# Optimization experiments

Hardware: AMD Instinct MI355X
Metric: run time of the kernel (lower is better)

Reference implementation:

```python
import jax, jax.numpy as jnp
import numpy as np
from jax import lax


def _conv3x3(x, w, b):
    # x: [B,C,H,W], w: [O,I,3,3] -> SAME padding, stride 1 (matches nn.Conv2d(.,.,3,1,1))
    y = lax.conv_general_dilated(x, w, window_strides=(1, 1), padding='SAME',
                                 dimension_numbers=('NCHW', 'OIHW', 'NCHW'))
    return y + b[None, :, None, None]


def _smooth_mask(h, w, dtype=jnp.float32):
    # Mirrors create_smooth_mask: torch.meshgrid(x, y, indexing='xy') -> shape (h, w),
    # xx varies along width, yy along height.
    yv = jnp.linspace(0.0, 1.0, h, dtype=dtype)   # height coords
    xv = jnp.linspace(0.0, 1.0, w, dtype=dtype)   # width coords
    xx = jnp.broadcast_to(xv[None, :], (h, w))
    yy = jnp.broadcast_to(yv[:, None], (h, w))
    edge_falloff = 0.1
    def edge(t):
        return jnp.minimum(jax.nn.sigmoid((t - edge_falloff) / 0.1),
                           jax.nn.sigmoid((1.0 - t - edge_falloff) / 0.1))
    return edge(xx) * edge(yy)  # (h, w); channel repeat handled by broadcasting


def _kaiming(key, shape):
    # kaiming_normal_(mode='fan_out', nonlinearity='relu'): std = sqrt(2 / fan_out)
    fan_out = shape[0] * shape[2] * shape[3]
    return jax.random.normal(key, shape, dtype=jnp.float32) * np.sqrt(2.0 / fan_out).astype(np.float32)


def setup_inputs() -> dict:
    key = jax.random.key(0)
    ks = jax.random.split(key, 6)
    B, H, W = 4, 720, 1280
    return {
        'frame1': jax.random.normal(ks[0], (B, 3, H, W), dtype=jnp.float32),
        'frame3': jax.random.normal(ks[1], (B, 3, H, W), dtype=jnp.float32),
        'w1': _kaiming(ks[2], (32, 6, 3, 3)),  'b1': jnp.zeros((32,), jnp.float32),
        'w2': _kaiming(ks[3], (48, 32, 3, 3)), 'b2': jnp.zeros((48,), jnp.float32),
        'w3': _kaiming(ks[4], (32, 48, 3, 3)), 'b3': jnp.zeros((32,), jnp.float32),
        'w4': _kaiming(ks[5], (3, 32, 3, 3)),  'b4': jnp.zeros((3,), jnp.float32),
    }


def reference(frame1, frame3, w1, b1, w2, b2, w3, b3, w4, b4):
    # For these inputs the detected motion region is the full frame for every
    # batch element (see notes), so the per-region loop batches into one pass.
    B, C, H, W = frame1.shape
    avg = (frame1 + frame3) * 0.5
    x = jnp.concatenate([frame1, frame3], axis=1)          # [B,6,H,W]
    h = jax.nn.relu(_conv3x3(x, w1, b1))                   # [B,32,H,W]
    h = jax.nn.relu(_conv3x3(h, w2, b2))                   # [B,48,H,W]
    h = jax.nn.relu(_conv3x3(h, w3, b3))                   # [B,32,H,W]
    region_out = _conv3x3(h, w4, b4)                       # [B,3,H,W]
    mask = _smooth_mask(H, W, frame1.dtype)[None, None]    # [1,1,H,W]
    out = avg * (1.0 - mask) + region_out * mask
    return jnp.clip(out, -1.0, 1.0)
```

## Files before the change

kernel.cpp:

```cpp
#include <hip/hip_runtime.h>

#define BATCH 4
#define H 720
#define W 1280
#define HW (H*W)

typedef _Float16 f16x8 __attribute__((ext_vector_type(8)));
typedef __attribute__((ext_vector_type(4))) float f32x4;

#define WP1_B 0
#define WP2_B 8192
#define WP3A_B 40960
#define WP3B_B 61440
#define WP4_B 81920
#define WP_BYTES 98304

__device__ __forceinline__ ushort f2h(float x) {
    union { _Float16 h; ushort u; } c; c.h = (_Float16)x; return c.u;
}

__global__ void pack_x_kernel(const float* __restrict__ f1, const float* __restrict__ f3,
                              ushort* __restrict__ X,
                              int xr0, int rows_x, int xbase, int RBX) {
    int p = blockIdx.x * 256 + threadIdx.x;
    int npix = BATCH * rows_x * W;
    if (p >= npix) return;
    int b = p / (rows_x * W);
    int rem = p - b * (rows_x * W);
    int ri = rem / W;
    int col = rem - ri * W;
    int img_row = xr0 + ri;
    int buf_row = img_row - xbase;
    const float* p1 = f1 + (size_t)b * 3 * HW + (size_t)img_row * W + col;
    const float* p3 = f3 + (size_t)b * 3 * HW + (size_t)img_row * W + col;
    union { ushort u[8]; uint4 v; } r;
    r.u[0] = f2h(p1[0]);  r.u[1] = f2h(p1[HW]);  r.u[2] = f2h(p1[2*HW]);
    r.u[3] = f2h(p3[0]);  r.u[4] = f2h(p3[HW]);  r.u[5] = f2h(p3[2*HW]);
    r.u[6] = 0; r.u[7] = 0;
    *reinterpret_cast<uint4*>(X + (((size_t)b * RBX + buf_row) * W + col) * 8) = r.v;
}

__global__ void pack_w_kernel(const float* __restrict__ w1, const float* __restrict__ w2,
                              const float* __restrict__ w3, const float* __restrict__ w4,
                              ushort* __restrict__ wp1, ushort* __restrict__ wp2,
                              ushort* __restrict__ wp3a, ushort* __restrict__ wp3b,
                              ushort* __restrict__ wp4) {
    int i = blockIdx.x * 256 + threadIdx.x;
    if (i < 3072) {
        int j = i & 7, l = (i >> 3) & 63, f = i >> 9;
        int dy = f >> 1, mt = f & 1;
        int dx = l >> 4, ci = j, och = mt * 16 + (l & 15);
        float v = 0.f;
        if (dx < 3 && ci < 6) v = w1[((och * 6 + ci) * 3 + dy) * 3 + dx];
        wp1[i] = f2h(v);
        return;
    }
    i -= 3072;
    if (i < 13824) {
        int j = i & 7, l = (i >> 3) & 63, f = i >> 9;
        int tap = f / 3, mt = f - tap * 3;
        int dy = tap / 3, dx = tap - dy * 3;
        int och = mt * 16 + (l & 15), ci = (l >> 4) * 8 + j;
        wp2[i] = f2h(w2[((och * 32 + ci) * 3 + dy) * 3 + dx]);
        return;
    }
    i -= 13824;
    if (i < 9216) {
        int j = i & 7, l = (i >> 3) & 63, f = i >> 9;
        int tap = f >> 1, mt = f & 1;
        int dy = tap / 3, dx = tap - dy * 3;
        int och = mt * 16 + (l & 15), ci = (l >> 4) * 8 + j;
        wp3a[i] = f2h(w3[((och * 48 + ci) * 3 + dy) * 3 + dx]);
        return;
    }
    i -= 9216;
    if (i < 9216) {
        int j = i & 7, l = (i >> 3) & 63, f = i >> 9;
        int tap = f >> 1, mt = f & 1;
        int dy = tap / 3, dx = tap - dy * 3;
        int och = mt * 16 + (l & 15), ci = 32 + (l >> 4) * 8 + j;
        float v = 0.f;
        if (ci < 48) v = w3[((och * 48 + ci) * 3 + dy) * 3 + dx];
        wp3b[i] = f2h(v);
        return;
    }
    i -= 9216;
    if (i < 4608) {
        int j = i & 7, l = (i >> 3) & 63, tap = i >> 9;
        int dy = tap / 3, dx = tap - dy * 3;
        int och = l & 15, ci = (l >> 4) * 8 + j;
        float v = 0.f;
        if (och < 3) v = w4[((och * 32 + ci) * 3 + dy) * 3 + dx];
        wp4[i] = f2h(v);
    }
}

__device__ __forceinline__ void lds_copy(const unsigned char* __restrict__ g, char* s, int bytes) {
    const uint4* gs = reinterpret_cast<const uint4*>(g);
    uint4* ss = reinterpret_cast<uint4*>(s);
    for (int i = threadIdx.x; i < bytes / 16; i += 256) ss[i] = gs[i];
    __syncthreads();
}

__global__ __launch_bounds__(256) void conv1_kernel(const ushort* __restrict__ Xg,
                                                    const float* __restrict__ bias,
                                                    ushort* __restrict__ Y,
                                                    const unsigned char* __restrict__ wp,
                                                    int y0, int xbase, int RBX, int y1base, int RBY1) {
    __shared__ char lds[6144];
    lds_copy(wp, lds, 6144);
    int wave = threadIdx.x >> 6, lane = threadIdx.x & 63;
    int l15 = lane & 15, lhi = lane >> 4;
    int y = y0 + blockIdx.y, b = blockIdx.z;
    int x0 = blockIdx.x * 256 + wave * 64;

    f32x4 acc[2][4] = {};
    #pragma unroll
    for (int dy = 0; dy < 3; ++dy) {
        int yy = y + dy - 1;
        bool rv = (yy >= 0 && yy < H);
        size_t srow = ((size_t)b * RBX + (yy - xbase)) * W;
        f16x8 bfrag[4];
        #pragma unroll
        for (int nt = 0; nt < 4; ++nt) {
            int xc = x0 + nt * 16 + l15 + lhi - 1;
            uint4 v = make_uint4(0, 0, 0, 0);
            if (rv && lhi < 3 && xc >= 0 && xc < W)
                v = *reinterpret_cast<const uint4*>(Xg + (srow + xc) * 8);
            bfrag[nt] = *reinterpret_cast<f16x8*>(&v);
        }
        #pragma unroll
        for (int mt = 0; mt < 2; ++mt) {
            f16x8 a = *reinterpret_cast<f16x8*>(lds + ((dy * 2 + mt) * 64 + lane) * 16);
            #pragma unroll
            for (int nt = 0; nt < 4; ++nt)
                acc[mt][nt] = __builtin_amdgcn_mfma_f32_16x16x32_f16(a, bfrag[nt], acc[mt][nt], 0, 0, 0);
        }
    }
    size_t drow = ((size_t)b * RBY1 + (y - y1base)) * W;
    #pragma unroll
    for (int mt = 0; mt < 2; ++mt) {
        float4 bs = *reinterpret_cast<const float4*>(bias + mt * 16 + lhi * 4);
        const float* bsp = reinterpret_cast<const float*>(&bs);
        #pragma unroll
        for (int nt = 0; nt < 4; ++nt) {
            size_t pix = drow + x0 + nt * 16 + l15;
            ushort o[4];
            #pragma unroll
            for (int r = 0; r < 4; ++r) o[r] = f2h(fmaxf(acc[mt][nt][r] + bsp[r], 0.f));
            *reinterpret_cast<uint2*>(Y + pix * 32 + mt * 16 + lhi * 4) = *reinterpret_cast<uint2*>(o);
        }
    }
}

__global__ __launch_bounds__(256) void conv2_kernel(const ushort* __restrict__ Y1,
                                                    const float* __restrict__ bias,
                                                    ushort* __restrict__ Y2,
                                                    const unsigned char* __restrict__ wp,
                                                    int y0, int y1base, int RBY1, int y2base, int RBY2) {
    __shared__ char lds[27648];
    lds_copy(wp, lds, 27648);
    int wave = threadIdx.x >> 6, lane = threadIdx.x & 63;
    int l15 = lane & 15, lhi = lane >> 4;
    int y = y0 + blockIdx.y, b = blockIdx.z;
    int x0 = blockIdx.x * 256 + wave * 64;

    f32x4 acc[3][4] = {};
    #pragma unroll
    for (int dy = 0; dy < 3; ++dy) {
        int yy = y + dy - 1;
        bool rv = (yy >= 0 && yy < H);
        size_t srow = ((size_t)b * RBY1 + (yy - y1base)) * W;
        #pragma unroll
        for (int dx = 0; dx < 3; ++dx) {
            int tap = dy * 3 + dx;
            f16x8 bfrag[4];
            #pragma unroll
            for (int nt = 0; nt < 4; ++nt) {
                int xc = x0 + nt * 16 + l15 + dx - 1;
                uint4 v = make_uint4(0, 0, 0, 0);
                if (rv && xc >= 0 && xc < W)
                    v = *reinterpret_cast<const uint4*>(Y1 + (srow + xc) * 32 + lhi * 8);
                bfrag[nt] = *reinterpret_cast<f16x8*>(&v);
            }
            #pragma unroll
            for (int mt = 0; mt < 3; ++mt) {
                f16x8 a = *reinterpret_cast<f16x8*>(lds + ((tap * 3 + mt) * 64 + lane) * 16);
                #pragma unroll
                for (int nt = 0; nt < 4; ++nt)
                    acc[mt][nt] = __builtin_amdgcn_mfma_f32_16x16x32_f16(a, bfrag[nt], acc[mt][nt], 0, 0, 0);
            }
        }
    }
    size_t drow = ((size_t)b * RBY2 + (y - y2base)) * W;
    #pragma unroll
    for (int mt = 0; mt < 3; ++mt) {
        float4 bs = *reinterpret_cast<const float4*>(bias + mt * 16 + lhi * 4);
        const float* bsp = reinterpret_cast<const float*>(&bs);
        #pragma unroll
        for (int nt = 0; nt < 4; ++nt) {
            size_t pix = drow + x0 + nt * 16 + l15;
            ushort o[4];
            #pragma unroll
            for (int r = 0; r < 4; ++r) o[r] = f2h(fmaxf(acc[mt][nt][r] + bsp[r], 0.f));
            *reinterpret_cast<uint2*>(Y2 + pix * 48 + mt * 16 + lhi * 4) = *reinterpret_cast<uint2*>(o);
        }
    }
}

__global__ __launch_bounds__(256) void conv3_kernel(const ushort* __restrict__ Y2,
                                                    const float* __restrict__ bias,
                                                    ushort* __restrict__ Y3,
                                                    const unsigned char* __restrict__ wpa,
                                                    const unsigned char* __restrict__ wpb,
                                                    int y0, int y2base, int RBY2, int y3base, int RBY3) {
    __shared__ char lds[36864];
    {
        const uint4* ga = reinterpret_cast<const uint4*>(wpa);
        const uint4* gb = reinterpret_cast<const uint4*>(wpb);
        uint4* ss = reinterpret_cast<uint4*>(lds);
        for (int i = threadIdx.x; i < 18432 / 16; i += 256) { ss[i] = ga[i]; ss[i + 1152] = gb[i]; }
        __syncthreads();
    }
    int wave = threadIdx.x >> 6, lane = threadIdx.x & 63;
    int l15 = lane & 15, lhi = lane >> 4;
    int y = y0 + blockIdx.y, b = blockIdx.z;
    int x0 = blockIdx.x * 256 + wave * 64;

    f32x4 acc[2][4] = {};
    #pragma unroll
    for (int dy = 0; dy < 3; ++dy) {
        int yy = y + dy - 1;
        bool rv = (yy >= 0 && yy < H);
        size_t srow = ((size_t)b * RBY2 + (yy - y2base)) * W;
        #pragma unroll
        for (int dx = 0; dx < 3; ++dx) {
            int tap = dy * 3 + dx;
            f16x8 b0[4], b1[4];
            #pragma unroll
            for (int nt = 0; nt < 4; ++nt) {
                int xc = x0 + nt * 16 + l15 + dx - 1;
                bool valid = rv && xc >= 0 && xc < W;
                uint4 v0 = make_uint4(0, 0, 0, 0), v1 = make_uint4(0, 0, 0, 0);
                if (valid)
                    v0 = *reinterpret_cast<const uint4*>(Y2 + (srow + xc) * 48 + lhi * 8);
                if (valid && lhi < 2)
                    v1 = *reinterpret_cast<const uint4*>(Y2 + (srow + xc) * 48 + 32 + lhi * 8);
                b0[nt] = *reinterpret_cast<f16x8*>(&v0);
                b1[nt] = *reinterpret_cast<f16x8*>(&v1);
            }
            #pragma unroll
            for (int mt = 0; mt < 2; ++mt) {
                f16x8 a0 = *reinterpret_cast<f16x8*>(lds + ((tap * 2 + mt) * 64 + lane) * 16);
                f16x8 a1 = *reinterpret_cast<f16x8*>(lds + 18432 + ((tap * 2 + mt) * 64 + lane) * 16);
                #pragma unroll
                for (int nt = 0; nt < 4; ++nt) {
                    acc[mt][nt] = __builtin_amdgcn_mfma_f32_16x16x32_f16(a0, b0[nt], acc[mt][nt], 0, 0, 0);
                    acc[mt][nt] = __builtin_amdgcn_mfma_f32_16x16x32_f16(a1, b1[nt], acc[mt][nt], 0, 0, 0);
                }
            }
        }
    }
    size_t drow = ((size_t)b * RBY3 + (y - y3base)) * W;
    #pragma unroll
    for (int mt = 0; mt < 2; ++mt) {
        float4 bs = *reinterpret_cast<const float4*>(bias + mt * 16 + lhi * 4);
        const float* bsp = reinterpret_cast<const float*>(&bs);
        #pragma unroll
        for (int nt = 0; nt < 4; ++nt) {
            size_t pix = drow + x0 + nt * 16 + l15;
            ushort o[4];
            #pragma unroll
            for (int r = 0; r < 4; ++r) o[r] = f2h(fmaxf(acc[mt][nt][r] + bsp[r], 0.f));
            *reinterpret_cast<uint2*>(Y3 + pix * 32 + mt * 16 + lhi * 4) = *reinterpret_cast<uint2*>(o);
        }
    }
}

__device__ __forceinline__ float edgef(float t) {
    float a = 1.f / (1.f + expf(-(t - 0.1f) * 10.f));
    float c = 1.f / (1.f + expf(-(0.9f - t) * 10.f));
    return fminf(a, c);
}

__global__ __launch_bounds__(256) void conv4_kernel(const ushort* __restrict__ Y3,
                                                    const float* __restrict__ b4,
                                                    const float* __restrict__ f1,
                                                    const float* __restrict__ f3,
                                                    float* __restrict__ out,
                                                    const unsigned char* __restrict__ wp,
                                                    int y0, int y3base, int RBY3) {
    __shared__ char lds[9216];
    lds_copy(wp, lds, 9216);
    int wave = threadIdx.x >> 6, lane = threadIdx.x & 63;
    int l15 = lane & 15, lhi = lane >> 4;
    int y = y0 + blockIdx.y, b = blockIdx.z;
    int x0 = blockIdx.x * 256 + wave * 64;

    f32x4 acc[4] = {};
    #pragma unroll
    for (int dy = 0; dy < 3; ++dy) {
        int yy = y + dy - 1;
        bool rv = (yy >= 0 && yy < H);
        size_t srow = ((size_t)b * RBY3 + (yy - y3base)) * W;
        #pragma unroll
        for (int dx = 0; dx < 3; ++dx) {
            int tap = dy * 3 + dx;
            f16x8 bfrag[4];
            #pragma unroll
            for (int nt = 0; nt < 4; ++nt) {
                int xc = x0 + nt * 16 + l15 + dx - 1;
                uint4 v = make_uint4(0, 0, 0, 0);
                if (rv && xc >= 0 && xc < W)
                    v = *reinterpret_cast<const uint4*>(Y3 + (srow + xc) * 32 + lhi * 8);
                bfrag[nt] = *reinterpret_cast<f16x8*>(&v);
            }
            f16x8 a = *reinterpret_cast<f16x8*>(lds + (tap * 64 + lane) * 16);
            #pragma unroll
            for (int nt = 0; nt < 4; ++nt)
                acc[nt] = __builtin_amdgcn_mfma_f32_16x16x32_f16(a, bfrag[nt], acc[nt], 0, 0, 0);
        }
    }
    if (lhi == 0) {
        float bv0 = b4[0], bv1 = b4[1], bv2 = b4[2];
        float ty = (float)y * (1.f / (H - 1));
        float ey = edgef(ty);
        #pragma unroll
        for (int nt = 0; nt < 4; ++nt) {
            int x = x0 + nt * 16 + l15;
            float tx = (float)x * (1.f / (W - 1));
            float m = edgef(tx) * ey;
            float om = 1.f - m;
            #pragma unroll
            for (int r = 0; r < 3; ++r) {
                float bv = (r == 0) ? bv0 : (r == 1 ? bv1 : bv2);
                size_t idx = ((size_t)(b * 3 + r) * H + y) * W + x;
                float avg = 0.5f * (f1[idx] + f3[idx]);
                float v = avg * om + (acc[nt][r] + bv) * m;
                out[idx] = fminf(fmaxf(v, -1.f), 1.f);
            }
        }
    }
}

extern "C" void kernel_launch(void* const* d_in, const int* in_sizes, int n_in,
                              void* d_out, int out_size, void* d_ws, size_t ws_size,
                              hipStream_t stream) {
    const float* f1 = (const float*)d_in[0];
    const float* f3 = (const float*)d_in[1];
    const float* w1 = (const float*)d_in[2];
    const float* b1 = (const float*)d_in[3];
    const float* w2 = (const float*)d_in[4];
    const float* b2 = (const float*)d_in[5];
    const float* w3 = (const float*)d_in[6];
    const float* b3 = (const float*)d_in[7];
    const float* w4 = (const float*)d_in[8];
    const float* b4 = (const float*)d_in[9];
    float* out = (float*)d_out;

    long avail = (long)ws_size - 131072;
    int RB = -1;
    for (int nb = 1; nb <= 180; ++nb) {
        int rb = (H + nb - 1) / nb;
        long need = 10240L * (120L * rb + 512);
        if (need <= avail) { RB = rb; break; }
    }
    if (RB < 0) return;

    int RBX = RB + 8, RBY1 = RB + 6, RBY2 = RB + 4, RBY3 = RB + 2;
    char* ws = (char*)d_ws;
    size_t offX  = 0;
    size_t offY1 = offX  + (size_t)BATCH * RBX  * W * 8  * 2;
    size_t offY2 = offY1 + (size_t)BATCH * RBY1 * W * 32 * 2;
    size_t offY3 = offY2 + (size_t)BATCH * RBY2 * W * 48 * 2;
    size_t offWP = offY3 + (size_t)BATCH * RBY3 * W * 32 * 2;
    ushort* X  = (ushort*)(ws + offX);
    ushort* Y1 = (ushort*)(ws + offY1);
    ushort* Y2 = (ushort*)(ws + offY2);
    ushort* Y3 = (ushort*)(ws + offY3);
    ushort* wp1  = (ushort*)(ws + offWP + WP1_B);
    ushort* wp2  = (ushort*)(ws + offWP + WP2_B);
    ushort* wp3a = (ushort*)(ws + offWP + WP3A_B);
    ushort* wp3b = (ushort*)(ws + offWP + WP3B_B);
    ushort* wp4  = (ushort*)(ws + offWP + WP4_B);

    pack_w_kernel<<<156, 256, 0, stream>>>(w1, w2, w3, w4, wp1, wp2, wp3a, wp3b, wp4);

    for (int r0 = 0; r0 < H; r0 += RB) {
        int r1 = r0 + RB; if (r1 > H) r1 = H;
        int xbase = r0 - 4, y1base = r0 - 3, y2base = r0 - 2, y3base = r0 - 1;

        int xr0 = r0 - 4 < 0 ? 0 : r0 - 4;
        int xr1 = r1 + 4 > H ? H : r1 + 4;
        int rows_x = xr1 - xr0;
        int npix = BATCH * rows_x * W;
        pack_x_kernel<<<(npix + 255) / 256, 256, 0, stream>>>(f1, f3, X, xr0, rows_x, xbase, RBX);

        int y10 = r0 - 3 < 0 ? 0 : r0 - 3;
        int y11 = r1 + 3 > H ? H : r1 + 3;
        conv1_kernel<<<dim3(W / 256, y11 - y10, BATCH), 256, 0, stream>>>(
            X, b1, Y1, (const unsigned char*)wp1, y10, xbase, RBX, y1base, RBY1);

        int y20 = r0 - 2 < 0 ? 0 : r0 - 2;
        int y21 = r1 + 2 > H ? H : r1 + 2;
        conv2_kernel<<<dim3(W / 256, y21 - y20, BATCH), 256, 0, stream>>>(
            Y1, b2, Y2, (const unsigned char*)wp2, y20, y1base, RBY1, y2base, RBY2);

        int y30 = r0 - 1 < 0 ? 0 : r0 - 1;
        int y31 = r1 + 1 > H ? H : r1 + 1;
        conv3_kernel<<<dim3(W / 256, y31 - y30, BATCH), 256, 0, stream>>>(
            Y2, b3, Y3, (const unsigned char*)wp3a, (const unsigned char*)wp3b,
            y30, y2base, RBY2, y3base, RBY3);

        conv4_kernel<<<dim3(W / 256, r1 - r0, BATCH), 256, 0, stream>>>(
            Y3, b4, f1, f3, out, (const unsigned char*)wp4, r0, y3base, RBY3);
    }
}
```

Measured before the change: 938.8 us.

## Pad activation buffers with zero borders, remap workgroups per XCD, hoist tap loads

Activation buffers get explicit zero-padded columns, and out-of-image rows are written as zeros. The conv kernels can then drop per-tap bounds checks and branchy loads and use plain vector loads from a single base pointer. Workgroups are flattened into a 1D grid and remapped so that contiguous work lands on the same XCD, which should improve L2 locality. Loads for all three dx taps are hoisted per dy row. The change adds a pad-zeroing kernel, extra rows of compute at the image edges, and higher register pressure from the hoisted fragments.

```diff
diff --git a/kernel.cpp b/kernel.cpp
--- a/kernel.cpp
+++ b/kernel.cpp
@@ -4,14 +4,15 @@
 #define H 720
 #define W 1280
 #define HW (H*W)
+#define WX (W+4)
+#define WP (W+2)
 
 typedef _Float16 f16x8 __attribute__((ext_vector_type(8)));
 typedef __attribute__((ext_vector_type(4))) float f32x4;
 
 #define WP1_B 0
 #define WP2_B 8192
-#define WP3A_B 40960
-#define WP3B_B 61440
+#define WP3_B 40960
 #define WP4_B 81920
 #define WP_BYTES 98304
 
@@ -19,32 +20,80 @@
     union { _Float16 h; ushort u; } c; c.h = (_Float16)x; return c.u;
 }
 
+__device__ __forceinline__ int xcd_work(int id, int nwg) {
+    int q = nwg >> 3, r = nwg & 7;
+    int k = id & 7, i = id >> 3;
+    int extra = k < r ? k : r;
+    return k * q + extra + i;
+}
+
+__global__ void zero_pads_kernel(ushort* __restrict__ X, ushort* __restrict__ Y1,
+                                 ushort* __restrict__ Y2, ushort* __restrict__ Y3,
+                                 int RBX, int RBY1, int RBY2, int RBY3) {
+    int i = blockIdx.x * 256 + threadIdx.x;
+    uint4 z = make_uint4(0, 0, 0, 0);
+    int nX = BATCH * RBX * 4;
+    if (i < nX) {
+        int c4 = i & 3, row = i >> 2;
+        int col = (c4 == 0) ? 0 : (W + c4);
+        *reinterpret_cast<uint4*>(X + ((size_t)row * WX + col) * 8) = z;
+        return;
+    }
+    i -= nX;
+    int n1 = BATCH * RBY1 * 2;
+    if (i < n1) {
+        int c = i & 1, row = i >> 1;
+        int col = c ? (W + 1) : 0;
+        uint4* p = reinterpret_cast<uint4*>(Y1 + ((size_t)row * WP + col) * 32);
+        p[0] = z; p[1] = z; p[2] = z; p[3] = z;
+        return;
+    }
+    i -= n1;
+    int n2 = BATCH * RBY2 * 2;
+    if (i < n2) {
+        int c = i & 1, row = i >> 1;
+        int col = c ? (W + 1) : 0;
+        uint4* p = reinterpret_cast<uint4*>(Y2 + ((size_t)row * WP + col) * 48);
+        p[0] = z; p[1] = z; p[2] = z; p[3] = z; p[4] = z; p[5] = z;
+        return;
+    }
+    i -= n2;
+    int n3 = BATCH * RBY3 * 2;
+    if (i < n3) {
+        int c = i & 1, row = i >> 1;
+        int col = c ? (W + 1) : 0;
+        uint4* p = reinterpret_cast<uint4*>(Y3 + ((size_t)row * WP + col) * 32);
+        p[0] = z; p[1] = z; p[2] = z; p[3] = z;
+    }
+}
+
 __global__ void pack_x_kernel(const float* __restrict__ f1, const float* __restrict__ f3,
-                              ushort* __restrict__ X,
-                              int xr0, int rows_x, int xbase, int RBX) {
+                              ushort* __restrict__ X, int xbase, int RBX) {
     int p = blockIdx.x * 256 + threadIdx.x;
-    int npix = BATCH * rows_x * W;
+    int npix = BATCH * RBX * W;
     if (p >= npix) return;
-    int b = p / (rows_x * W);
-    int rem = p - b * (rows_x * W);
+    int b = p / (RBX * W);
+    int rem = p - b * (RBX * W);
     int ri = rem / W;
     int col = rem - ri * W;
-    int img_row = xr0 + ri;
-    int buf_row = img_row - xbase;
-    const float* p1 = f1 + (size_t)b * 3 * HW + (size_t)img_row * W + col;
-    const float* p3 = f3 + (size_t)b * 3 * HW + (size_t)img_row * W + col;
+    int img_row = xbase + ri;
     union { ushort u[8]; uint4 v; } r;
-    r.u[0] = f2h(p1[0]);  r.u[1] = f2h(p1[HW]);  r.u[2] = f2h(p1[2*HW]);
-    r.u[3] = f2h(p3[0]);  r.u[4] = f2h(p3[HW]);  r.u[5] = f2h(p3[2*HW]);
-    r.u[6] = 0; r.u[7] = 0;
-    *reinterpret_cast<uint4*>(X + (((size_t)b * RBX + buf_row) * W + col) * 8) = r.v;
+    if (img_row >= 0 && img_row < H) {
+        const float* p1 = f1 + (size_t)b * 3 * HW + (size_t)img_row * W + col;
+        const float* p3 = f3 + (size_t)b * 3 * HW + (size_t)img_row * W + col;
+        r.u[0] = f2h(p1[0]);  r.u[1] = f2h(p1[HW]);  r.u[2] = f2h(p1[2*HW]);
+        r.u[3] = f2h(p3[0]);  r.u[4] = f2h(p3[HW]);  r.u[5] = f2h(p3[2*HW]);
+        r.u[6] = 0; r.u[7] = 0;
+    } else {
+        r.v = make_uint4(0, 0, 0, 0);
+    }
+    *reinterpret_cast<uint4*>(X + (((size_t)b * RBX + ri) * WX + col + 1) * 8) = r.v;
 }
 
 __global__ void pack_w_kernel(const float* __restrict__ w1, const float* __restrict__ w2,
                               const float* __restrict__ w3, const float* __restrict__ w4,
                               ushort* __restrict__ wp1, ushort* __restrict__ wp2,
-                              ushort* __restrict__ wp3a, ushort* __restrict__ wp3b,
-                              ushort* __restrict__ wp4) {
+                              ushort* __restrict__ wp3, ushort* __restrict__ wp4) {
     int i = blockIdx.x * 256 + threadIdx.x;
     if (i < 3072) {
         int j = i & 7, l = (i >> 3) & 63, f = i >> 9;
@@ -70,7 +119,7 @@
         int tap = f >> 1, mt = f & 1;
         int dy = tap / 3, dx = tap - dy * 3;
         int och = mt * 16 + (l & 15), ci = (l >> 4) * 8 + j;
-        wp3a[i] = f2h(w3[((och * 48 + ci) * 3 + dy) * 3 + dx]);
+        wp3[i] = f2h(w3[((och * 48 + ci) * 3 + dy) * 3 + dx]);
         return;
     }
     i -= 9216;
@@ -81,7 +130,7 @@
         int och = mt * 16 + (l & 15), ci = 32 + (l >> 4) * 8 + j;
         float v = 0.f;
         if (ci < 48) v = w3[((och * 48 + ci) * 3 + dy) * 3 + dx];
-        wp3b[i] = f2h(v);
+        wp3[9216 + i] = f2h(v);
         return;
     }
     i -= 9216;
@@ -106,29 +155,26 @@
                                                     const float* __restrict__ bias,
                                                     ushort* __restrict__ Y,
                                                     const unsigned char* __restrict__ wp,
-                                                    int y0, int xbase, int RBX, int y1base, int RBY1) {
+                                                    int y0, int ny, int xbase, int RBX,
+                                                    int y1base, int RBY1) {
     __shared__ char lds[6144];
     lds_copy(wp, lds, 6144);
     int wave = threadIdx.x >> 6, lane = threadIdx.x & 63;
     int l15 = lane & 15, lhi = lane >> 4;
-    int y = y0 + blockIdx.y, b = blockIdx.z;
-    int x0 = blockIdx.x * 256 + wave * 64;
+    int work = xcd_work(blockIdx.x, gridDim.x);
+    int bx = work % 5, t = work / 5, by = t % ny, b = t / ny;
+    int y = y0 + by;
+    int x0 = bx * 256 + wave * 64;
+    bool zrow = (y < 0) | (y >= H);
 
     f32x4 acc[2][4] = {};
     #pragma unroll
     for (int dy = 0; dy < 3; ++dy) {
-        int yy = y + dy - 1;
-        bool rv = (yy >= 0 && yy < H);
-        size_t srow = ((size_t)b * RBX + (yy - xbase)) * W;
+        const ushort* rp = Xg + (((size_t)b * RBX + (y + dy - 1 - xbase)) * WX + x0 + l15 + lhi) * 8;
         f16x8 bfrag[4];
         #pragma unroll
-        for (int nt = 0; nt < 4; ++nt) {
-            int xc = x0 + nt * 16 + l15 + lhi - 1;
-            uint4 v = make_uint4(0, 0, 0, 0);
-            if (rv && lhi < 3 && xc >= 0 && xc < W)
-                v = *reinterpret_cast<const uint4*>(Xg + (srow + xc) * 8);
-            bfrag[nt] = *reinterpret_cast<f16x8*>(&v);
-        }
+        for (int nt = 0; nt < 4; ++nt)
+            bfrag[nt] = *reinterpret_cast<const f16x8*>(rp + nt * 128);
         #pragma unroll
         for (int mt = 0; mt < 2; ++mt) {
             f16x8 a = *reinterpret_cast<f16x8*>(lds + ((dy * 2 + mt) * 64 + lane) * 16);
@@ -137,18 +183,18 @@
                 acc[mt][nt] = __builtin_amdgcn_mfma_f32_16x16x32_f16(a, bfrag[nt], acc[mt][nt], 0, 0, 0);
         }
     }
-    size_t drow = ((size_t)b * RBY1 + (y - y1base)) * W;
+    ushort* wpx = Y + (((size_t)b * RBY1 + (y - y1base)) * WP + x0 + l15 + 1) * 32 + lhi * 4;
     #pragma unroll
     for (int mt = 0; mt < 2; ++mt) {
         float4 bs = *reinterpret_cast<const float4*>(bias + mt * 16 + lhi * 4);
         const float* bsp = reinterpret_cast<const float*>(&bs);
         #pragma unroll
         for (int nt = 0; nt < 4; ++nt) {
-            size_t pix = drow + x0 + nt * 16 + l15;
             ushort o[4];
             #pragma unroll
-            for (int r = 0; r < 4; ++r) o[r] = f2h(fmaxf(acc[mt][nt][r] + bsp[r], 0.f));
-            *reinterpret_cast<uint2*>(Y + pix * 32 + mt * 16 + lhi * 4) = *reinterpret_cast<uint2*>(o);
+            for (int r = 0; r < 4; ++r)
+                o[r] = zrow ? (ushort)0 : f2h(fmaxf(acc[mt][nt][r] + bsp[r], 0.f));
+            *reinterpret_cast<uint2*>(wpx + nt * 512 + mt * 16) = *reinterpret_cast<uint2*>(o);
         }
     }
 }
@@ -157,53 +203,51 @@
                                                     const float* __restrict__ bias,
                                                     ushort* __restrict__ Y2,
                                                     const unsigned char* __restrict__ wp,
-                                                    int y0, int y1base, int RBY1, int y2base, int RBY2) {
+                                                    int y0, int ny, int y1base, int RBY1,
+                                                    int y2base, int RBY2) {
     __shared__ char lds[27648];
     lds_copy(wp, lds, 27648);
     int wave = threadIdx.x >> 6, lane = threadIdx.x & 63;
     int l15 = lane & 15, lhi = lane >> 4;
-    int y = y0 + blockIdx.y, b = blockIdx.z;
-    int x0 = blockIdx.x * 256 + wave * 64;
+    int work = xcd_work(blockIdx.x, gridDim.x);
+    int bx = work % 5, t = work / 5, by = t % ny, b = t / ny;
+    int y = y0 + by;
+    int x0 = bx * 256 + wave * 64;
+    bool zrow = (y < 0) | (y >= H);
+    int c0 = x0 + l15;
 
     f32x4 acc[3][4] = {};
     #pragma unroll
     for (int dy = 0; dy < 3; ++dy) {
-        int yy = y + dy - 1;
-        bool rv = (yy >= 0 && yy < H);
-        size_t srow = ((size_t)b * RBY1 + (yy - y1base)) * W;
-        #pragma unroll
-        for (int dx = 0; dx < 3; ++dx) {
-            int tap = dy * 3 + dx;
-            f16x8 bfrag[4];
-            #pragma unroll
-            for (int nt = 0; nt < 4; ++nt) {
-                int xc = x0 + nt * 16 + l15 + dx - 1;
-                uint4 v = make_uint4(0, 0, 0, 0);
-                if (rv && xc >= 0 && xc < W)
-                    v = *reinterpret_cast<const uint4*>(Y1 + (srow + xc) * 32 + lhi * 8);
-                bfrag[nt] = *reinterpret_cast<f16x8*>(&v);
-            }
+        const ushort* rp = Y1 + (((size_t)b * RBY1 + (y + dy - 1 - y1base)) * WP + c0) * 32 + lhi * 8;
+        f16x8 bf[3][4];
+        #pragma unroll
+        for (int nt = 0; nt < 4; ++nt)
+            #pragma unroll
+            for (int dx = 0; dx < 3; ++dx)
+                bf[dx][nt] = *reinterpret_cast<const f16x8*>(rp + nt * 512 + dx * 32);
+        #pragma unroll
+        for (int dx = 0; dx < 3; ++dx)
             #pragma unroll
             for (int mt = 0; mt < 3; ++mt) {
-                f16x8 a = *reinterpret_cast<f16x8*>(lds + ((tap * 3 + mt) * 64 + lane) * 16);
+                f16x8 a = *reinterpret_cast<f16x8*>(lds + (((dy * 3 + dx) * 3 + mt) * 64 + lane) * 16);
                 #pragma unroll
                 for (int nt = 0; nt < 4; ++nt)
-                    acc[mt][nt] = __builtin_amdgcn_mfma_f32_16x16x32_f16(a, bfrag[nt], acc[mt][nt], 0, 0, 0);
-            }
-        }
-    }
-    size_t drow = ((size_t)b * RBY2 + (y - y2base)) * W;
+                    acc[mt][nt] = __builtin_amdgcn_mfma_f32_16x16x32_f16(a, bf[dx][nt], acc[mt][nt], 0, 0, 0);
+            }
+    }
+    ushort* wpx = Y2 + (((size_t)b * RBY2 + (y - y2base)) * WP + x0 + l15 + 1) * 48 + lhi * 4;
     #pragma unroll
     for (int mt = 0; mt < 3; ++mt) {
         float4 bs = *reinterpret_cast<const float4*>(bias + mt * 16 + lhi * 4);
         const float* bsp = reinterpret_cast<const float*>(&bs);
         #pragma unroll
         for (int nt = 0; nt < 4; ++nt) {
-            size_t pix = drow + x0 + nt * 16 + l15;
             ushort o[4];
             #pragma unroll
-            for (int r = 0; r < 4; ++r) o[r] = f2h(fmaxf(acc[mt][nt][r] + bsp[r], 0.f));
-            *reinterpret_cast<uint2*>(Y2 + pix * 48 + mt * 16 + lhi * 4) = *reinterpret_cast<uint2*>(o);
+            for (int r = 0; r < 4; ++r)
+                o[r] = zrow ? (ushort)0 : f2h(fmaxf(acc[mt][nt][r] + bsp[r], 0.f));
+            *reinterpret_cast<uint2*>(wpx + nt * 768 + mt * 16) = *reinterpret_cast<uint2*>(o);
         }
     }
 }
@@ -211,68 +255,71 @@
 __global__ __launch_bounds__(256) void conv3_kernel(const ushort* __restrict__ Y2,
                                                     const float* __restrict__ bias,
                                                     ushort* __restrict__ Y3,
-                                                    const unsigned char* __restrict__ wpa,
-                                                    const unsigned char* __restrict__ wpb,
-                                                    int y0, int y2base, int RBY2, int y3base, int RBY3) {
+                                                    const unsigned char* __restrict__ wp,
+                                                    int y0, int ny, int y2base, int RBY2,
+                                                    int y3base, int RBY3) {
     __shared__ char lds[36864];
-    {
-        const uint4* ga = reinterpret_cast<const uint4*>(wpa);
-        const uint4* gb = reinterpret_cast<const uint4*>(wpb);
-        uint4* ss = reinterpret_cast<uint4*>(lds);
-        for (int i = threadIdx.x; i < 18432 / 16; i += 256) { ss[i] = ga[i]; ss[i + 1152] = gb[i]; }
-        __syncthreads();
-    }
+    lds_copy(wp, lds, 36864);
     int wave = threadIdx.x >> 6, lane = threadIdx.x & 63;
     int l15 = lane & 15, lhi = lane >> 4;
-    int y = y0 + blockIdx.y, b = blockIdx.z;
-    int x0 = blockIdx.x * 256 + wave * 64;
+    int work = xcd_work(blockIdx.x, gridDim.x);
+    int bx = work % 5, t = work / 5, by = t % ny, b = t / ny;
+    int y = y0 + by;
+    int x0 = bx * 256 + wave * 64;
+    bool zrow = (y < 0) | (y >= H);
+    int c0 = x0 + l15;
 
     f32x4 acc[2][4] = {};
     #pragma unroll
     for (int dy = 0; dy < 3; ++dy) {
-        int yy = y + dy - 1;
-        bool rv = (yy >= 0 && yy < H);
-        size_t srow = ((size_t)b * RBY2 + (yy - y2base)) * W;
-        #pragma unroll
-        for (int dx = 0; dx < 3; ++dx) {
-            int tap = dy * 3 + dx;
-            f16x8 b0[4], b1[4];
-            #pragma unroll
-            for (int nt = 0; nt < 4; ++nt) {
-                int xc = x0 + nt * 16 + l15 + dx - 1;
-                bool valid = rv && xc >= 0 && xc < W;
-                uint4 v0 = make_uint4(0, 0, 0, 0), v1 = make_uint4(0, 0, 0, 0);
-                if (valid)
-                    v0 = *reinterpret_cast<const uint4*>(Y2 + (srow + xc) * 48 + lhi * 8);
-                if (valid && lhi < 2)
-                    v1 = *reinterpret_cast<const uint4*>(Y2 + (srow + xc) * 48 + 32 + lhi * 8);
-                b0[nt] = *reinterpret_cast<f16x8*>(&v0);
-                b1[nt] = *reinterpret_cast<f16x8*>(&v1);
-            }
+        const ushort* rp = Y2 + (((size_t)b * RBY2 + (y + dy - 1 - y2base)) * WP + c0) * 48 + lhi * 8;
+        const ushort* rp2 = rp + 1536;
+        f16x8 bf[3][4];
+        #pragma unroll
+        for (int nt = 0; nt < 2; ++nt)
+            #pragma unroll
+            for (int dx = 0; dx < 3; ++dx) {
+                bf[dx][nt]     = *reinterpret_cast<const f16x8*>(rp  + nt * 768 + dx * 48);
+                bf[dx][nt + 2] = *reinterpret_cast<const f16x8*>(rp2 + nt * 768 + dx * 48);
+            }
+        #pragma unroll
+        for (int dx = 0; dx < 3; ++dx)
             #pragma unroll
             for (int mt = 0; mt < 2; ++mt) {
-                f16x8 a0 = *reinterpret_cast<f16x8*>(lds + ((tap * 2 + mt) * 64 + lane) * 16);
-                f16x8 a1 = *reinterpret_cast<f16x8*>(lds + 18432 + ((tap * 2 + mt) * 64 + lane) * 16);
+                f16x8 a = *reinterpret_cast<f16x8*>(lds + (((dy * 3 + dx) * 2 + mt) * 64 + lane) * 16);
                 #pragma unroll
-                for (int nt = 0; nt < 4; ++nt) {
-                    acc[mt][nt] = __builtin_amdgcn_mfma_f32_16x16x32_f16(a0, b0[nt], acc[mt][nt], 0, 0, 0);
-                    acc[mt][nt] = __builtin_amdgcn_mfma_f32_16x16x32_f16(a1, b1[nt], acc[mt][nt], 0, 0, 0);
-                }
-            }
-        }
-    }
-    size_t drow = ((size_t)b * RBY3 + (y - y3base)) * W;
+                for (int nt = 0; nt < 4; ++nt)
+                    acc[mt][nt] = __builtin_amdgcn_mfma_f32_16x16x32_f16(a, bf[dx][nt], acc[mt][nt], 0, 0, 0);
+            }
+        #pragma unroll
+        for (int nt = 0; nt < 2; ++nt)
+            #pragma unroll
+            for (int dx = 0; dx < 3; ++dx) {
+                bf[dx][nt]     = *reinterpret_cast<const f16x8*>(rp  + nt * 768 + dx * 48 + 32);
+                bf[dx][nt + 2] = *reinterpret_cast<const f16x8*>(rp2 + nt * 768 + dx * 48 + 32);
+            }
+        #pragma unroll
+        for (int dx = 0; dx < 3; ++dx)
+            #pragma unroll
+            for (int mt = 0; mt < 2; ++mt) {
+                f16x8 a = *reinterpret_cast<f16x8*>(lds + 18432 + (((dy * 3 + dx) * 2 + mt) * 64 + lane) * 16);
+                #pragma unroll
+                for (int nt = 0; nt < 4; ++nt)
+                    acc[mt][nt] = __builtin_amdgcn_mfma_f32_16x16x32_f16(a, bf[dx][nt], acc[mt][nt], 0, 0, 0);
+            }
+    }
+    ushort* wpx = Y3 + (((size_t)b * RBY3 + (y - y3base)) * WP + x0 + l15 + 1) * 32 + lhi * 4;
     #pragma unroll
     for (int mt = 0; mt < 2; ++mt) {
         float4 bs = *reinterpret_cast<const float4*>(bias + mt * 16 + lhi * 4);
         const float* bsp = reinterpret_cast<const float*>(&bs);
         #pragma unroll
         for (int nt = 0; nt < 4; ++nt) {
-            size_t pix = drow + x0 + nt * 16 + l15;
             ushort o[4];
             #pragma unroll
-            for (int r = 0; r < 4; ++r) o[r] = f2h(fmaxf(acc[mt][nt][r] + bsp[r], 0.f));
-            *reinterpret_cast<uint2*>(Y3 + pix * 32 + mt * 16 + lhi * 4) = *reinterpret_cast<uint2*>(o);
+            for (int r = 0; r < 4; ++r)
+                o[r] = zrow ? (ushort)0 : f2h(fmaxf(acc[mt][nt][r] + bsp[r], 0.f));
+            *reinterpret_cast<uint2*>(wpx + nt * 512 + mt * 16) = *reinterpret_cast<uint2*>(o);
         }
     }
 }
@@ -289,36 +336,33 @@
                                                     const float* __restrict__ f3,
                                                     float* __restrict__ out,
                                                     const unsigned char* __restrict__ wp,
-                                                    int y0, int y3base, int RBY3) {
+                                                    int y0, int ny, int y3base, int RBY3) {
     __shared__ char lds[9216];
     lds_copy(wp, lds, 9216);
     int wave = threadIdx.x >> 6, lane = threadIdx.x & 63;
     int l15 = lane & 15, lhi = lane >> 4;
-    int y = y0 + blockIdx.y, b = blockIdx.z;
-    int x0 = blockIdx.x * 256 + wave * 64;
+    int work = xcd_work(blockIdx.x, gridDim.x);
+    int bx = work % 5, t = work / 5, by = t % ny, b = t / ny;
+    int y = y0 + by;
+    int x0 = bx * 256 + wave * 64;
+    int c0 = x0 + l15;
 
     f32x4 acc[4] = {};
     #pragma unroll
     for (int dy = 0; dy < 3; ++dy) {
-        int yy = y + dy - 1;
-        bool rv = (yy >= 0 && yy < H);
-        size_t srow = ((size_t)b * RBY3 + (yy - y3base)) * W;
+        const ushort* rp = Y3 + (((size_t)b * RBY3 + (y + dy - 1 - y3base)) * WP + c0) * 32 + lhi * 8;
+        f16x8 bf[3][4];
+        #pragma unroll
+        for (int nt = 0; nt < 4; ++nt)
+            #pragma unroll
+            for (int dx = 0; dx < 3; ++dx)
+                bf[dx][nt] = *reinterpret_cast<const f16x8*>(rp + nt * 512 + dx * 32);
         #pragma unroll
         for (int dx = 0; dx < 3; ++dx) {
-            int tap = dy * 3 + dx;
-            f16x8 bfrag[4];
-            #pragma unroll
-            for (int nt = 0; nt < 4; ++nt) {
-                int xc = x0 + nt * 16 + l15 + dx - 1;
-                uint4 v = make_uint4(0, 0, 0, 0);
-                if (rv && xc >= 0 && xc < W)
-                    v = *reinterpret_cast<const uint4*>(Y3 + (srow + xc) * 32 + lhi * 8);
-                bfrag[nt] = *reinterpret_cast<f16x8*>(&v);
-            }
-            f16x8 a = *reinterpret_cast<f16x8*>(lds + (tap * 64 + lane) * 16);
+            f16x8 a = *reinterpret_cast<f16x8*>(lds + ((dy * 3 + dx) * 64 + lane) * 16);
             #pragma unroll
             for (int nt = 0; nt < 4; ++nt)
-                acc[nt] = __builtin_amdgcn_mfma_f32_16x16x32_f16(a, bfrag[nt], acc[nt], 0, 0, 0);
+                acc[nt] = __builtin_amdgcn_mfma_f32_16x16x32_f16(a, bf[dx][nt], acc[nt], 0, 0, 0);
         }
     }
     if (lhi == 0) {
@@ -358,61 +402,55 @@
     const float* b4 = (const float*)d_in[9];
     float* out = (float*)d_out;
 
-    long avail = (long)ws_size - 131072;
     int RB = -1;
     for (int nb = 1; nb <= 180; ++nb) {
         int rb = (H + nb - 1) / nb;
-        long need = 10240L * (120L * rb + 512);
-        if (need <= avail) { RB = rb; break; }
+        long need = 1230848L * rb + 5252096L + 131072L;
+        if (need <= (long)ws_size) { RB = rb; break; }
     }
     if (RB < 0) return;
 
     int RBX = RB + 8, RBY1 = RB + 6, RBY2 = RB + 4, RBY3 = RB + 2;
     char* ws = (char*)d_ws;
     size_t offX  = 0;
-    size_t offY1 = offX  + (size_t)BATCH * RBX  * W * 8  * 2;
-    size_t offY2 = offY1 + (size_t)BATCH * RBY1 * W * 32 * 2;
-    size_t offY3 = offY2 + (size_t)BATCH * RBY2 * W * 48 * 2;
-    size_t offWP = offY3 + (size_t)BATCH * RBY3 * W * 32 * 2;
+    size_t offY1 = offX  + (size_t)BATCH * RBX  * WX * 8  * 2;
+    size_t offY2 = offY1 + (size_t)BATCH * RBY1 * WP * 32 * 2;
+    size_t offY3 = offY2 + (size_t)BATCH * RBY2 * WP * 48 * 2;
+    size_t offWPr = offY3 + (size_t)BATCH * RBY3 * WP * 32 * 2;
     ushort* X  = (ushort*)(ws + offX);
     ushort* Y1 = (ushort*)(ws + offY1);
     ushort* Y2 = (ushort*)(ws + offY2);
     ushort* Y3 = (ushort*)(ws + offY3);
-    ushort* wp1  = (ushort*)(ws + offWP + WP1_B);
-    ushort* wp2  = (ushort*)(ws + offWP + WP2_B);
-    ushort* wp3a = (ushort*)(ws + offWP + WP3A_B);
-    ushort* wp3b = (ushort*)(ws + offWP + WP3B_B);
-    ushort* wp4  = (ushort*)(ws + offWP + WP4_B);
-
-    pack_w_kernel<<<156, 256, 0, stream>>>(w1, w2, w3, w4, wp1, wp2, wp3a, wp3b, wp4);
+    ushort* wp1 = (ushort*)(ws + offWPr + WP1_B);
+    ushort* wp2 = (ushort*)(ws + offWPr + WP2_B);
+    ushort* wp3 = (ushort*)(ws + offWPr + WP3_B);
+    ushort* wp4 = (ushort*)(ws + offWPr + WP4_B);
+
+    pack_w_kernel<<<156, 256, 0, stream>>>(w1, w2, w3, w4, wp1, wp2, wp3, wp4);
+    int npad = BATCH * (RBX * 4 + (RBY1 + RBY2 + RBY3) * 2);
+    zero_pads_kernel<<<(npad + 255) / 256, 256, 0, stream>>>(X, Y1, Y2, Y3, RBX, RBY1, RBY2, RBY3);
 
     for (int r0 = 0; r0 < H; r0 += RB) {
         int r1 = r0 + RB; if (r1 > H) r1 = H;
         int xbase = r0 - 4, y1base = r0 - 3, y2base = r0 - 2, y3base = r0 - 1;
 
-        int xr0 = r0 - 4 < 0 ? 0 : r0 - 4;
-        int xr1 = r1 + 4 > H ? H : r1 + 4;
-        int rows_x = xr1 - xr0;
-        int npix = BATCH * rows_x * W;
-        pack_x_kernel<<<(npix + 255) / 256, 256, 0, stream>>>(f1, f3, X, xr0, rows_x, xbase, RBX);
-
-        int y10 = r0 - 3 < 0 ? 0 : r0 - 3;
-        int y11 = r1 + 3 > H ? H : r1 + 3;
-        conv1_kernel<<<dim3(W / 256, y11 - y10, BATCH), 256, 0, stream>>>(
-            X, b1, Y1, (const unsigned char*)wp1, y10, xbase, RBX, y1base, RBY1);
-
-        int y20 = r0 - 2 < 0 ? 0 : r0 - 2;
-        int y21 = r1 + 2 > H ? H : r1 + 2;
-        conv2_kernel<<<dim3(W / 256, y21 - y20, BATCH), 256, 0, stream>>>(
-            Y1, b2, Y2, (const unsigned char*)wp2, y20, y1base, RBY1, y2base, RBY2);
-
-        int y30 = r0 - 1 < 0 ? 0 : r0 - 1;
-        int y31 = r1 + 1 > H ? H : r1 + 1;
-        conv3_kernel<<<dim3(W / 256, y31 - y30, BATCH), 256, 0, stream>>>(
-            Y2, b3, Y3, (const unsigned char*)wp3a, (const unsigned char*)wp3b,
-            y30, y2base, RBY2, y3base, RBY3);
-
-        conv4_kernel<<<dim3(W / 256, r1 - r0, BATCH), 256, 0, stream>>>(
-            Y3, b4, f1, f3, out, (const unsigned char*)wp4, r0, y3base, RBY3);
-    }
-}
+        int npix = BATCH * RBX * W;
+        pack_x_kernel<<<(npix + 255) / 256, 256, 0, stream>>>(f1, f3, X, xbase, RBX);
+
+        int ny1 = (r1 + 3) - (r0 - 3);
+        conv1_kernel<<<5 * ny1 * BATCH, 256, 0, stream>>>(
+            X, b1, Y1, (const unsigned char*)wp1, r0 - 3, ny1, xbase, RBX, y1base, RBY1);
+
+        int ny2 = (r1 + 2) - (r0 - 2);
+        conv2_kernel<<<5 * ny2 * BATCH, 256, 0, stream>>>(
+            Y1, b2, Y2, (const unsigned char*)wp2, r0 - 2, ny2, y1base, RBY1, y2base, RBY2);
+
+        int ny3 = (r1 + 1) - (r0 - 1);
+        conv3_kernel<<<5 * ny3 * BATCH, 256, 0, stream>>>(
+            Y2, b3, Y3, (const unsigned char*)wp3, r0 - 1, ny3, y2base, RBY2, y3base, RBY3);
+
+        int ny4 = r1 - r0;
+        conv4_kernel<<<5 * ny4 * BATCH, 256, 0, stream>>>(
+            Y3, b4, f1, f3, out, (const unsigned char*)wp4, r0, ny4, y3base, RBY3);
+    }
+}
```

Result: faster. 910.5 us (-3.0%).
